# Kernel optimization log

Measured on AMD Instinct MI355X. Metric: run time of the kernel, lower is better.

Reference implementation:

```python
import jax, jax.numpy as jnp
import numpy as np

TEMP = 0.05
EPS = 1e-8  # F.cosine_similarity eps

def setup_inputs() -> dict:
    key = jax.random.key(0)
    k1, k2 = jax.random.split(key)
    cls = jax.random.normal(k1, (4096, 1024), dtype=jnp.float32)
    hidden = jax.random.normal(k2, (4096, 1024), dtype=jnp.float32)
    return {"cls": cls, "hidden": hidden}

def _normalize(x):
    # matches F.cosine_similarity: divide by max(||x||, eps)
    n = jnp.sqrt(jnp.sum(x * x, axis=-1, keepdims=True))
    return x / jnp.maximum(n, EPS)

def reference(cls, hidden):
    a = _normalize(cls)          # [B, H]
    b = _normalize(hidden)       # [B, H]
    sim = jnp.einsum('ih,jh->ij', a, b) / TEMP  # [B, B] cosine sims / temp
    # cross-entropy with labels = arange(B): mean(logsumexp(row) - diag)
    lse = jax.nn.logsumexp(sim, axis=-1)        # [B]
    diag = jnp.diagonal(sim)                    # [B]
    return jnp.mean(lse - diag)
```

## Files before the change

kernel.cpp:

```cpp
#include <hip/hip_runtime.h>
#include <hip/hip_bf16.h>

typedef __attribute__((ext_vector_type(8))) short bf16x8;
typedef __attribute__((ext_vector_type(4))) float f32x4;

#define B_ROWS 4096
#define H_DIM  1024
#define TEMP_INV 20.0f
#define BM 256
#define BK 64
#define NT (H_DIM / BK)

__device__ __forceinline__ void gload_lds16(const void* g, void* l) {
  __builtin_amdgcn_global_load_lds(
      (const __attribute__((address_space(1))) void*)g,
      (__attribute__((address_space(3))) void*)l, 16, 0, 0);
}

__global__ __launch_bounds__(256) void normalize_kernel(
    const float* __restrict__ cls, const float* __restrict__ hid,
    __hip_bfloat16* __restrict__ Abf, __hip_bfloat16* __restrict__ Bbf,
    float* __restrict__ rowsum)
{
  int bid = blockIdx.x, tid = threadIdx.x;
  if (bid < 16) rowsum[bid * 256 + tid] = 0.0f;
  int row = bid & (B_ROWS - 1);
  const float* src = (bid < B_ROWS) ? cls : hid;
  __hip_bfloat16* dst = (bid < B_ROWS) ? Abf : Bbf;

  float4 v = reinterpret_cast<const float4*>(src + (size_t)row * H_DIM)[tid];
  float ss = v.x * v.x + v.y * v.y + v.z * v.z + v.w * v.w;
  #pragma unroll
  for (int off = 1; off < 64; off <<= 1) ss += __shfl_xor(ss, off, 64);
  __shared__ float wsum[4];
  if ((tid & 63) == 0) wsum[tid >> 6] = ss;
  __syncthreads();
  float total = wsum[0] + wsum[1] + wsum[2] + wsum[3];
  float scale = 1.0f / fmaxf(sqrtf(total), 1e-8f);

  union { ushort4 u; __hip_bfloat16 h[4]; } o;
  o.h[0] = __float2bfloat16(v.x * scale);
  o.h[1] = __float2bfloat16(v.y * scale);
  o.h[2] = __float2bfloat16(v.z * scale);
  o.h[3] = __float2bfloat16(v.w * scale);
  reinterpret_cast<ushort4*>(dst + (size_t)row * H_DIM)[tid] = o.u;
}


#define LDS_RD_A(BUF, MB)                                                     \
  { _Pragma("unroll") for (int mi = 0; mi < 4; mi++) {                        \
      _Pragma("unroll") for (int ks = 0; ks < 2; ks++) {                      \
        af[mi][ks] = *(const bf16x8*)(&As[BUF][(rA2 ^ (ks << 6)) + ((MB) + mi) * 2048]); } } }

#define LDS_RD_B(BUF, NB)                                                     \
  { _Pragma("unroll") for (int ni = 0; ni < 2; ni++) {                        \
      _Pragma("unroll") for (int ks = 0; ks < 2; ks++) {                      \
        bfr[(NB) + ni][ks] = *(const bf16x8*)(&Bs[BUF][(rB2 ^ (ks << 6)) + ((NB) + ni) * 2048]); } } }

#define MFMA16(MB, NB)                                                        \
  { __builtin_amdgcn_s_setprio(1);                                            \
    _Pragma("unroll") for (int mi = 0; mi < 4; mi++) {                        \
      _Pragma("unroll") for (int ni = 0; ni < 2; ni++) {                      \
        _Pragma("unroll") for (int ks = 0; ks < 2; ks++) {                    \
          acc[(MB) + mi][(NB) + ni] = __builtin_amdgcn_mfma_f32_16x16x32_bf16(\
              af[mi][ks], bfr[(NB) + ni][ks], acc[(MB) + mi][(NB) + ni], 0, 0, 0); } } } \
    __builtin_amdgcn_s_setprio(0); }

#define BARB() __builtin_amdgcn_s_barrier()
#define WAITK()                                                               \
  { asm volatile("s_waitcnt lgkmcnt(0)" ::: "memory");                        \
    __builtin_amdgcn_sched_barrier(0); }

#define STAGE_A(BUF, TT, C)                                                   \
  gload_lds16(Abase + (size_t)(row0 + (C) * 64 + srow) * 2048 + (TT) * 128 + scolb, \
              &As[BUF][(C) * 8192 + tid * 16])
#define STAGE_B(BUF, TT, C)                                                   \
  gload_lds16(Bbase + (size_t)(col0 + (C) * 64 + srow) * 2048 + (TT) * 128 + scolb, \
              &Bs[BUF][(C) * 8192 + tid * 16])

#define KTILE(BUF, T_)                                                        \
  { const int Tn = (T_) + 1;                                                  \
                                         \
    LDS_RD_A(BUF, 0);                                                         \
    if (Tn < NT) { STAGE_A(BUF ^ 1, Tn, 2); STAGE_A(BUF ^ 1, Tn, 3); }        \
    BARB(); WAITK(); MFMA16(0, 0); BARB();                                    \
                                         \
    LDS_RD_B(BUF, 2);                                                         \
    if (Tn < NT) { STAGE_B(BUF ^ 1, Tn, 0); STAGE_B(BUF ^ 1, Tn, 1); }        \
    BARB(); WAITK(); MFMA16(0, 2); BARB();                                    \
                                         \
    LDS_RD_A(BUF, 4);                                                         \
    if (Tn < NT) { STAGE_B(BUF ^ 1, Tn, 2); STAGE_B(BUF ^ 1, Tn, 3); }        \
    BARB(); WAITK(); MFMA16(4, 0); BARB();                                    \
           \
    if ((T_) + 2 < NT) {                                                      \
      STAGE_A(BUF, (T_) + 2, 0); STAGE_A(BUF, (T_) + 2, 1);                   \
      asm volatile("s_waitcnt vmcnt(2)" ::: "memory");                        \
    } else if (Tn < NT) {                                                     \
      asm volatile("s_waitcnt vmcnt(0)" ::: "memory");                        \
    }                                                                         \
    BARB();                                                                   \
    if (Tn < NT) { LDS_RD_B(BUF ^ 1, 0); }                                    \
    MFMA16(4, 2); BARB(); }

__global__ __launch_bounds__(512, 2) void gemm_kernel(
    const __hip_bfloat16* __restrict__ A, const __hip_bfloat16* __restrict__ Bm,
    float* __restrict__ rowsum, float* __restrict__ diag)
{
  __shared__ __align__(16) char As[2][32768];
  __shared__ __align__(16) char Bs[2][32768];

  const int tid  = threadIdx.x;
  const int lane = tid & 63;
  const int w    = tid >> 6;
  const int wm   = w >> 2, wn = w & 3;
  const int bm = blockIdx.y, bn = blockIdx.x;
  const long row0 = (long)bm * BM, col0 = (long)bn * BM;
  const char* Abase = (const char*)A;
  const char* Bbase = (const char*)Bm;

  const int srow  = tid >> 3;
  const int scolb = ((tid & 7) ^ ((tid >> 3) & 7)) << 4;

  const int dsw = (lane & 7) << 4;
  const int rA2 = (((wm * 128 + (lane & 15)) * 128) + ((lane >> 4) * 16)) ^ dsw;
  const int rB2 = (((wn * 64  + (lane & 15)) * 128) + ((lane >> 4) * 16)) ^ dsw;

  f32x4 acc[8][4] = {};
  bf16x8 af[4][2], bfr[4][2];

  #pragma unroll
  for (int c = 0; c < 4; c++) STAGE_A(0, 0, c);
  #pragma unroll
  for (int c = 0; c < 4; c++) STAGE_B(0, 0, c);
  STAGE_A(1, 1, 0); STAGE_A(1, 1, 1);
  asm volatile("s_waitcnt vmcnt(2)" ::: "memory");
  BARB();
  LDS_RD_B(0, 0);

  #pragma unroll 1
  for (int T = 0; T < NT; T += 2) {
    KTILE(0, T);
    KTILE(1, T + 1);
  }

  const bool isdiag = (bm == bn);
  const int g = lane >> 4;
  #pragma unroll
  for (int m = 0; m < 8; m++) {
    const int rowb = (int)row0 + wm * 128 + m * 16 + g * 4;
    float p[4] = {0.f, 0.f, 0.f, 0.f};
    #pragma unroll
    for (int n = 0; n < 4; n++) {
      const int colb = (int)col0 + wn * 64 + n * 16 + (lane & 15);
      #pragma unroll
      for (int r = 0; r < 4; r++) {
        float sim = acc[m][n][r] * TEMP_INV;
        if (isdiag && (rowb + r == colb)) diag[rowb + r] = sim;
        p[r] += __expf(sim);
      }
    }
    #pragma unroll
    for (int r = 0; r < 4; r++) {
      float s = p[r];
      s += __shfl_xor(s, 1, 64);
      s += __shfl_xor(s, 2, 64);
      s += __shfl_xor(s, 4, 64);
      s += __shfl_xor(s, 8, 64);
      if ((lane & 15) == 0) atomicAdd(&rowsum[rowb + r], s);
    }
  }
}

__global__ __launch_bounds__(1024) void finalize_kernel(
    const float* __restrict__ rowsum, const float* __restrict__ diag,
    float* __restrict__ out)
{
  int tid = threadIdx.x;
  float acc = 0.f;
  for (int i = tid; i < B_ROWS; i += 1024)
    acc += logf(rowsum[i]) - diag[i];
  #pragma unroll
  for (int off = 1; off < 64; off <<= 1) acc += __shfl_xor(acc, off, 64);
  __shared__ float wsum[16];
  if ((tid & 63) == 0) wsum[tid >> 6] = acc;
  __syncthreads();
  if (tid == 0) {
    float t = 0.f;
    #pragma unroll
    for (int i = 0; i < 16; i++) t += wsum[i];
    out[0] = t * (1.0f / B_ROWS);
  }
}

extern "C" void kernel_launch(void* const* d_in, const int* in_sizes, int n_in,
                              void* d_out, int out_size, void* d_ws, size_t ws_size,
                              hipStream_t stream)
{
  const float* cls = (const float*)d_in[0];
  const float* hid = (const float*)d_in[1];
  float* out = (float*)d_out;
  char* ws = (char*)d_ws;

  __hip_bfloat16* Abf = (__hip_bfloat16*)ws;
  __hip_bfloat16* Bbf = (__hip_bfloat16*)(ws + (size_t)B_ROWS * H_DIM * 2);
  float* rowsum = (float*)(ws + (size_t)B_ROWS * H_DIM * 4);
  float* diag   = rowsum + B_ROWS;

  hipLaunchKernelGGL(normalize_kernel, dim3(2 * B_ROWS), dim3(256), 0, stream,
                     cls, hid, Abf, Bbf, rowsum);
  hipLaunchKernelGGL(gemm_kernel, dim3(B_ROWS / BM, B_ROWS / BM), dim3(512), 0, stream,
                     Abf, Bbf, rowsum, diag);
  hipLaunchKernelGGL(finalize_kernel, dim3(1), dim3(1024), 0, stream,
                     rowsum, diag, out);
}
```

Baseline: 120.8 us.

## Replace global atomics with per-block partial row sums; one wave per row in normalize

The GEMM epilogue no longer issues global atomicAdds into a rowsum array. Each tile now reduces its exp-sums across waves in LDS and writes one partial per row into a [16 x 4096] buffer, which the finalize kernel sums before taking the log. This removes atomic contention and the zero-initialisation dependency. The normalize kernel is also restructured so each wavefront handles a whole row with a shuffle-only reduction and no block barrier, and fewer blocks are launched. The cost is an extra LDS pass and barrier in the GEMM, plus a single-block finalize that now reads sixteen times as much data.

```diff
diff --git a/kernel.cpp b/kernel.cpp
--- a/kernel.cpp
+++ b/kernel.cpp
@@ -10,6 +10,7 @@
 #define BM 256
 #define BK 64
 #define NT (H_DIM / BK)
+#define NBN (B_ROWS / BM)
 
 __device__ __forceinline__ void gload_lds16(const void* g, void* l) {
   __builtin_amdgcn_global_load_lds(
@@ -19,31 +20,34 @@
 
 __global__ __launch_bounds__(256) void normalize_kernel(
     const float* __restrict__ cls, const float* __restrict__ hid,
-    __hip_bfloat16* __restrict__ Abf, __hip_bfloat16* __restrict__ Bbf,
-    float* __restrict__ rowsum)
-{
-  int bid = blockIdx.x, tid = threadIdx.x;
-  if (bid < 16) rowsum[bid * 256 + tid] = 0.0f;
-  int row = bid & (B_ROWS - 1);
-  const float* src = (bid < B_ROWS) ? cls : hid;
-  __hip_bfloat16* dst = (bid < B_ROWS) ? Abf : Bbf;
-
-  float4 v = reinterpret_cast<const float4*>(src + (size_t)row * H_DIM)[tid];
-  float ss = v.x * v.x + v.y * v.y + v.z * v.z + v.w * v.w;
+    __hip_bfloat16* __restrict__ Abf, __hip_bfloat16* __restrict__ Bbf)
+{
+  const int w = threadIdx.x >> 6, lane = threadIdx.x & 63;
+  const int r = blockIdx.x * 4 + w;
+  const int rr = r & (B_ROWS - 1);
+  const float* src = ((r < B_ROWS) ? cls : hid) + (size_t)rr * H_DIM;
+  __hip_bfloat16* dst = ((r < B_ROWS) ? Abf : Bbf) + (size_t)rr * H_DIM;
+
+  float4 v[4];
+  float ss = 0.f;
+  #pragma unroll
+  for (int j = 0; j < 4; j++) {
+    v[j] = reinterpret_cast<const float4*>(src)[j * 64 + lane];
+    ss += v[j].x * v[j].x + v[j].y * v[j].y + v[j].z * v[j].z + v[j].w * v[j].w;
+  }
   #pragma unroll
   for (int off = 1; off < 64; off <<= 1) ss += __shfl_xor(ss, off, 64);
-  __shared__ float wsum[4];
-  if ((tid & 63) == 0) wsum[tid >> 6] = ss;
-  __syncthreads();
-  float total = wsum[0] + wsum[1] + wsum[2] + wsum[3];
-  float scale = 1.0f / fmaxf(sqrtf(total), 1e-8f);
-
-  union { ushort4 u; __hip_bfloat16 h[4]; } o;
-  o.h[0] = __float2bfloat16(v.x * scale);
-  o.h[1] = __float2bfloat16(v.y * scale);
-  o.h[2] = __float2bfloat16(v.z * scale);
-  o.h[3] = __float2bfloat16(v.w * scale);
-  reinterpret_cast<ushort4*>(dst + (size_t)row * H_DIM)[tid] = o.u;
+  const float scale = 1.0f / fmaxf(sqrtf(ss), 1e-8f);
+
+  #pragma unroll
+  for (int j = 0; j < 4; j++) {
+    union { ushort4 u; __hip_bfloat16 h[4]; } o;
+    o.h[0] = __float2bfloat16(v[j].x * scale);
+    o.h[1] = __float2bfloat16(v[j].y * scale);
+    o.h[2] = __float2bfloat16(v[j].z * scale);
+    o.h[3] = __float2bfloat16(v[j].w * scale);
+    reinterpret_cast<ushort4*>(dst)[j * 64 + lane] = o.u;
+  }
 }
 
 
@@ -80,19 +84,15 @@
 
 #define KTILE(BUF, T_)                                                        \
   { const int Tn = (T_) + 1;                                                  \
-                                         \
     LDS_RD_A(BUF, 0);                                                         \
     if (Tn < NT) { STAGE_A(BUF ^ 1, Tn, 2); STAGE_A(BUF ^ 1, Tn, 3); }        \
     BARB(); WAITK(); MFMA16(0, 0); BARB();                                    \
-                                         \
     LDS_RD_B(BUF, 2);                                                         \
     if (Tn < NT) { STAGE_B(BUF ^ 1, Tn, 0); STAGE_B(BUF ^ 1, Tn, 1); }        \
     BARB(); WAITK(); MFMA16(0, 2); BARB();                                    \
-                                         \
     LDS_RD_A(BUF, 4);                                                         \
     if (Tn < NT) { STAGE_B(BUF ^ 1, Tn, 2); STAGE_B(BUF ^ 1, Tn, 3); }        \
     BARB(); WAITK(); MFMA16(4, 0); BARB();                                    \
-           \
     if ((T_) + 2 < NT) {                                                      \
       STAGE_A(BUF, (T_) + 2, 0); STAGE_A(BUF, (T_) + 2, 1);                   \
       asm volatile("s_waitcnt vmcnt(2)" ::: "memory");                        \
@@ -105,7 +105,7 @@
 
 __global__ __launch_bounds__(512, 2) void gemm_kernel(
     const __hip_bfloat16* __restrict__ A, const __hip_bfloat16* __restrict__ Bm,
-    float* __restrict__ rowsum, float* __restrict__ diag)
+    float* __restrict__ pp, float* __restrict__ diag)
 {
   __shared__ __align__(16) char As[2][32768];
   __shared__ __align__(16) char Bs[2][32768];
@@ -146,6 +146,9 @@
 
   const bool isdiag = (bm == bn);
   const int g = lane >> 4;
+  __syncthreads();
+  float* lds_p = (float*)&As[0][0];
+
   #pragma unroll
   for (int m = 0; m < 8; m++) {
     const int rowb = (int)row0 + wm * 128 + m * 16 + g * 4;
@@ -167,19 +170,29 @@
       s += __shfl_xor(s, 2, 64);
       s += __shfl_xor(s, 4, 64);
       s += __shfl_xor(s, 8, 64);
-      if ((lane & 15) == 0) atomicAdd(&rowsum[rowb + r], s);
+      if ((lane & 15) == 0)
+        lds_p[wn * 256 + wm * 128 + m * 16 + g * 4 + r] = s;
     }
   }
+  __syncthreads();
+  if (tid < 256) {
+    float s = lds_p[tid] + lds_p[256 + tid] + lds_p[512 + tid] + lds_p[768 + tid];
+    pp[(size_t)bn * B_ROWS + row0 + tid] = s;
+  }
 }
 
 __global__ __launch_bounds__(1024) void finalize_kernel(
-    const float* __restrict__ rowsum, const float* __restrict__ diag,
+    const float* __restrict__ pp, const float* __restrict__ diag,
     float* __restrict__ out)
 {
   int tid = threadIdx.x;
   float acc = 0.f;
-  for (int i = tid; i < B_ROWS; i += 1024)
-    acc += logf(rowsum[i]) - diag[i];
+  for (int i = tid; i < B_ROWS; i += 1024) {
+    float s = 0.f;
+    #pragma unroll
+    for (int j = 0; j < NBN; j++) s += pp[(size_t)j * B_ROWS + i];
+    acc += logf(s) - diag[i];
+  }
   #pragma unroll
   for (int off = 1; off < 64; off <<= 1) acc += __shfl_xor(acc, off, 64);
   __shared__ float wsum[16];
@@ -204,13 +217,13 @@
 
   __hip_bfloat16* Abf = (__hip_bfloat16*)ws;
   __hip_bfloat16* Bbf = (__hip_bfloat16*)(ws + (size_t)B_ROWS * H_DIM * 2);
-  float* rowsum = (float*)(ws + (size_t)B_ROWS * H_DIM * 4);
-  float* diag   = rowsum + B_ROWS;
-
-  hipLaunchKernelGGL(normalize_kernel, dim3(2 * B_ROWS), dim3(256), 0, stream,
-                     cls, hid, Abf, Bbf, rowsum);
+  float* pp   = (float*)(ws + (size_t)B_ROWS * H_DIM * 4);
+  float* diag = pp + (size_t)NBN * B_ROWS;
+
+  hipLaunchKernelGGL(normalize_kernel, dim3(2 * B_ROWS / 4), dim3(256), 0, stream,
+                     cls, hid, Abf, Bbf);
   hipLaunchKernelGGL(gemm_kernel, dim3(B_ROWS / BM, B_ROWS / BM), dim3(512), 0, stream,
-                     Abf, Bbf, rowsum, diag);
+                     Abf, Bbf, pp, diag);
   hipLaunchKernelGGL(finalize_kernel, dim3(1), dim3(1024), 0, stream,
-                     rowsum, diag, out);
-}
+                     pp, diag, out);
+}
```

Measured after the change: 117.9 us. 2.4% less time.
